# Performance work log

Hardware: AMD Instinct MI355X
Metric: run time of the kernel (lower is better)

Reference implementation:

```python
import jax, jax.numpy as jnp
import numpy as np

HIDDEN = 4096
N_HEADS = 32
N_KV_HEADS = 8
HEAD_DIM = HIDDEN // N_HEADS  # 128
GROUPS = N_HEADS // N_KV_HEADS  # 4
B, S = 1, 2048
NEG = -1e9


def setup_inputs() -> dict:
    key = jax.random.key(0)
    ks = jax.random.split(key, 8)
    hidden_states = jax.random.normal(ks[0], (B, S, HIDDEN), dtype=jnp.float32)
    # additive causal mask [B,1,S,S]
    causal = jnp.tril(jnp.ones((S, S), dtype=bool))
    attention_mask = jnp.where(causal, 0.0, NEG).astype(jnp.float32)[None, None]
    position_ids = jnp.broadcast_to(jnp.arange(S, dtype=jnp.int64), (B, S))
    inv_freq = 1.0 / (500000.0 ** (np.arange(0, HEAD_DIM, 2, dtype=np.float32) / HEAD_DIM))
    freqs = np.arange(S, dtype=np.float32)[:, None] * inv_freq[None, :]  # [S, 64]
    cos = jnp.asarray(np.cos(freqs), dtype=jnp.float32)
    sin = jnp.asarray(np.sin(freqs), dtype=jnp.float32)
    sc = 1.0 / np.sqrt(HIDDEN)
    Wq = jax.random.normal(ks[1], (HIDDEN, HIDDEN), dtype=jnp.float32) * sc
    Wk = jax.random.normal(ks[2], (N_KV_HEADS * HEAD_DIM, HIDDEN), dtype=jnp.float32) * sc
    Wv = jax.random.normal(ks[3], (N_KV_HEADS * HEAD_DIM, HIDDEN), dtype=jnp.float32) * sc
    Wo = jax.random.normal(ks[4], (HIDDEN, HIDDEN), dtype=jnp.float32) * sc
    return {"hidden_states": hidden_states, "attention_mask": attention_mask,
            "position_ids": position_ids, "cos": cos, "sin": sin,
            "Wq": Wq, "Wk": Wk, "Wv": Wv, "Wo": Wo}


def _rope(q, k, cos, sin, position_ids):
    # cos/sin: [max_pos, head_dim//2]; gather per position -> [b,1,s,hd/2]
    c = cos[position_ids][:, None]  # [b,1,s,d/2]
    s_ = sin[position_ids][:, None]
    q1, q2 = q[..., ::2], q[..., 1::2]
    k1, k2 = k[..., ::2], k[..., 1::2]
    q_rot = jnp.concatenate([q1 * c - q2 * s_, q2 * c + q1 * s_], axis=-1)
    k_rot = jnp.concatenate([k1 * c - k2 * s_, k2 * c + k1 * s_], axis=-1)
    return q_rot, k_rot


def reference(hidden_states, attention_mask, position_ids, cos, sin, Wq, Wk, Wv, Wo):
    b, s, _ = hidden_states.shape
    q = jnp.einsum('bsh,oh->bso', hidden_states, Wq).reshape(b, s, N_HEADS, HEAD_DIM).transpose(0, 2, 1, 3)
    k = jnp.einsum('bsh,oh->bso', hidden_states, Wk).reshape(b, s, N_KV_HEADS, HEAD_DIM).transpose(0, 2, 1, 3)
    v = jnp.einsum('bsh,oh->bso', hidden_states, Wv).reshape(b, s, N_KV_HEADS, HEAD_DIM).transpose(0, 2, 1, 3)
    q, k = _rope(q, k, cos, sin, position_ids)
    if GROUPS > 1:
        k = jnp.repeat(k, GROUPS, axis=1)  # [b,H,s,d]
        v = jnp.repeat(v, GROUPS, axis=1)
    scores = jnp.einsum('bhqd,bhkd->bhqk', q, k) / np.sqrt(HEAD_DIM)
    scores = scores + attention_mask
    attn = jax.nn.softmax(scores.astype(jnp.float32), axis=-1).astype(q.dtype)
    out = jnp.einsum('bhqk,bhkd->bhqd', attn, v)
    out = out.transpose(0, 2, 1, 3).reshape(b, s, HIDDEN)
    out = jnp.einsum('bso,ho->bsh', out, Wo)
    return out
```

## Files before the change

kernel.cpp:

```cpp
#include <hip/hip_runtime.h>
#include <hip/hip_bf16.h>

#define S_LEN 2048
#define HID   4096
#define NH    32
#define NKV   8
#define HD    128

typedef __attribute__((ext_vector_type(8))) short short8v;
typedef __attribute__((ext_vector_type(4))) float floatx4;

__device__ __forceinline__ float bf2f(unsigned short u) {
  union { unsigned int u32; float f; } v; v.u32 = ((unsigned int)u) << 16; return v.f;
}
__device__ __forceinline__ unsigned short f2bf(float f) {
  union { float f; unsigned int u; } v; v.f = f;
  unsigned int u = v.u + 0x7fffu + ((v.u >> 16) & 1u);
  return (unsigned short)(u >> 16);
}
__device__ __forceinline__ unsigned int cvtpk_bf16(float lo, float hi) {
  unsigned int r;
  asm("v_cvt_pk_bf16_f32 %0, %1, %2" : "=v"(r) : "v"(lo), "v"(hi));
  return r;
}

__device__ __forceinline__ void gld_lds16(const void* g, void* l) {
  __builtin_amdgcn_global_load_lds((const __attribute__((address_space(1))) void*)g,
                                   (__attribute__((address_space(3))) void*)l, 16, 0, 0);
}

__global__ __launch_bounds__(256) void cvt_all(const float* __restrict__ X,  const float* __restrict__ Wq,
                                               const float* __restrict__ Wk, const float* __restrict__ Wv,
                                               const float* __restrict__ Wo,
                                               unsigned short* __restrict__ Xb,  unsigned short* __restrict__ Wqb,
                                               unsigned short* __restrict__ Wkb, unsigned short* __restrict__ Wvb,
                                               unsigned short* __restrict__ Wob) {
  const int c0 = 1048576;
  const int c1 = c0 + 2097152;
  const int c2 = c1 + 524288;
  const int c3 = c2 + 524288;
  const int c4 = c3 + 2097152;
  int i = blockIdx.x * blockDim.x + threadIdx.x;
  int stride = gridDim.x * blockDim.x;
  for (; i < c4; i += stride) {
    const float* src; unsigned short* dst; int off;
    if (i < c0)      { src = X;  dst = Xb;  off = i; }
    else if (i < c1) { src = Wq; dst = Wqb; off = i - c0; }
    else if (i < c2) { src = Wk; dst = Wkb; off = i - c1; }
    else if (i < c3) { src = Wv; dst = Wvb; off = i - c2; }
    else             { src = Wo; dst = Wob; off = i - c3; }
    float4 v0 = ((const float4*)src)[2 * off];
    float4 v1 = ((const float4*)src)[2 * off + 1];
    union { ushort4 h[2]; uint4 u; } o;
    o.h[0].x = f2bf(v0.x); o.h[0].y = f2bf(v0.y); o.h[0].z = f2bf(v0.z); o.h[0].w = f2bf(v0.w);
    o.h[1].x = f2bf(v1.x); o.h[1].y = f2bf(v1.y); o.h[1].z = f2bf(v1.z); o.h[1].w = f2bf(v1.w);
    ((uint4*)dst)[off] = o.u;
  }
}

__global__ __launch_bounds__(512, 2) void gemm_qkv(const unsigned short* __restrict__ Xb,
                                                   const unsigned short* __restrict__ Bcat,
                                                   unsigned short* __restrict__ Qg,
                                                   unsigned short* __restrict__ Kg,
                                                   unsigned short* __restrict__ Vt) {
  __shared__ unsigned short lds[2 * 16384 + 3 * 12288];
  const int K = 4096;
  const int tid = threadIdx.x;
  const int w = tid >> 6, lane = tid & 63;
  const int fr = lane & 15, fq = lane >> 4;
  const int wm = w >> 2, wn = w & 3;
  const int brow = blockIdx.y * 256, bcol = blockIdx.x * 192;

  const int r0s = w * 32 + (lane >> 2);
  const int r1s = r0s + 16;
  const int sl0 = ((lane & 3) ^ ((r0s >> 1) & 3)) << 3;
  const int sl1 = ((lane & 3) ^ ((r1s >> 1) & 3)) << 3;
  const unsigned short* pAs0 = Xb + (size_t)(brow + r0s) * K + sl0;
  const unsigned short* pAs1 = Xb + (size_t)(brow + r1s) * K + sl1;

  const unsigned short* pBs[3];
#pragma unroll
  for (int j = 0; j < 3; ++j) {
    int c = tid + j * 512;
    int khj = (c >= 768) ? 1 : 0;
    int rowj = (c - khj * 768) >> 2;
    int slotj = c & 3;
    pBs[j] = Bcat + (size_t)(bcol + rowj) * K + khj * 32 +
             ((slotj ^ ((rowj >> 1) & 3)) << 3);
  }

  const int sl = (fq ^ ((fr >> 1) & 3)) << 3;
  int aoffb[8], boffb[3];
#pragma unroll
  for (int m = 0; m < 8; ++m) aoffb[m] = (wm * 128 + m * 16 + fr) * 32 + sl;
#pragma unroll
  for (int n = 0; n < 3; ++n) boffb[n] = (wn * 48 + n * 16 + fr) * 32 + sl;

#define STG_A(buf, kh, t)                                                     \
  do {                                                                        \
    const int ko_ = (t) * 64 + (kh) * 32;                                     \
    gld_lds16(pAs0 + ko_, lds + (buf) * 16384 + (kh) * 8192 + w * 1024);      \
    gld_lds16(pAs1 + ko_, lds + (buf) * 16384 + (kh) * 8192 + w * 1024 + 512);\
  } while (0)
#define STG_B(bb, t)                                                          \
  do {                                                                        \
    const int ko_ = (t) * 64;                                                 \
    gld_lds16(pBs[0] + ko_, lds + 32768 + (bb) * 12288 + w * 512);            \
    gld_lds16(pBs[1] + ko_, lds + 32768 + (bb) * 12288 + 4096 + w * 512);     \
    gld_lds16(pBs[2] + ko_, lds + 32768 + (bb) * 12288 + 8192 + w * 512);     \
  } while (0)

  floatx4 acc[8][3] = {};

  STG_A(0, 0, 0); STG_A(0, 1, 0); STG_B(0, 0);
  STG_A(1, 0, 1);                 STG_B(1, 1);
  asm volatile("s_waitcnt vmcnt(5)" ::: "memory");
  __builtin_amdgcn_s_barrier();

  const int NT = K / 64;
  for (int t = 0; t < NT; ++t) {
    const int c = t & 1;
    const int bb = t % 3;
    const unsigned short* LA = lds + c * 16384;
    const unsigned short* LB = lds + 32768 + bb * 12288;
    short8v a_[8], b_[3];

#pragma unroll
    for (int m = 0; m < 8; ++m) a_[m] = *(const short8v*)&LA[aoffb[m]];
#pragma unroll
    for (int n = 0; n < 3; ++n) b_[n] = *(const short8v*)&LB[boffb[n]];
    if (t + 1 < NT) STG_A(c ^ 1, 1, t + 1);
    if (t + 2 < NT) STG_B((bb + 2) % 3, t + 2);
    __builtin_amdgcn_s_setprio(1);
#pragma unroll
    for (int m = 0; m < 8; ++m)
#pragma unroll
      for (int n = 0; n < 3; ++n)
        acc[m][n] = __builtin_amdgcn_mfma_f32_16x16x32_bf16(a_[m], b_[n], acc[m][n], 0, 0, 0);
    __builtin_amdgcn_s_setprio(0);
    if (t + 2 < NT)      asm volatile("s_waitcnt vmcnt(10)" ::: "memory");
    else if (t + 1 < NT) asm volatile("s_waitcnt vmcnt(7)" ::: "memory");
    else                 asm volatile("s_waitcnt vmcnt(0)" ::: "memory");
    __builtin_amdgcn_s_barrier();

#pragma unroll
    for (int m = 0; m < 8; ++m) a_[m] = *(const short8v*)&LA[8192 + aoffb[m]];
#pragma unroll
    for (int n = 0; n < 3; ++n) b_[n] = *(const short8v*)&LB[6144 + boffb[n]];
    if (t + 2 < NT) STG_A(c, 0, t + 2);
    __builtin_amdgcn_s_setprio(1);
#pragma unroll
    for (int m = 0; m < 8; ++m)
#pragma unroll
      for (int n = 0; n < 3; ++n)
        acc[m][n] = __builtin_amdgcn_mfma_f32_16x16x32_bf16(a_[m], b_[n], acc[m][n], 0, 0, 0);
    __builtin_amdgcn_s_setprio(0);
    if (t + 2 < NT)      asm volatile("s_waitcnt vmcnt(7)" ::: "memory");
    else if (t + 1 < NT) asm volatile("s_waitcnt vmcnt(2)" ::: "memory");
    else                 asm volatile("s_waitcnt vmcnt(0)" ::: "memory");
    __builtin_amdgcn_s_barrier();
  }
#undef STG_A
#undef STG_B

  const int r0 = brow + wm * 128 + fq * 4;
#pragma unroll
  for (int m = 0; m < 8; ++m)
#pragma unroll
    for (int n = 0; n < 3; ++n) {
      const int bc = bcol + wn * 48 + n * 16;
      if (bc < 4096) {
#pragma unroll
        for (int r = 0; r < 4; ++r)
          Qg[(size_t)(r0 + m * 16 + r) * HID + bc + fr] = f2bf(acc[m][n][r]);
      } else if (bc < 5120) {
#pragma unroll
        for (int r = 0; r < 4; ++r)
          Kg[(size_t)(r0 + m * 16 + r) * 1024 + bc - 4096 + fr] = f2bf(acc[m][n][r]);
      } else {
        ushort4 pk;
        pk.x = f2bf(acc[m][n][0]); pk.y = f2bf(acc[m][n][1]);
        pk.z = f2bf(acc[m][n][2]); pk.w = f2bf(acc[m][n][3]);
        *(ushort4*)&Vt[(size_t)(bc - 5120 + fr) * S_LEN + (r0 + m * 16)] = pk;
      }
    }
}

__global__ __launch_bounds__(512, 2) void gemm_o(const unsigned short* __restrict__ Ao,
                                                 const unsigned short* __restrict__ Wob,
                                                 float* __restrict__ Out) {
  __shared__ unsigned short lds[2 * 24576];
  const int K = 4096;
  const int tid = threadIdx.x;
  const int w = tid >> 6, lane = tid & 63;
  const int fr = lane & 15, fq = lane >> 4;
  const int wm = w >> 1, wn = w & 1;
  const int brow = blockIdx.y * 256, bcol = blockIdx.x * 128;

  const int rA = tid >> 2;
  const int sA = ((tid & 3) ^ ((rA >> 1) & 3)) << 3;
  const unsigned short* pA0 = Ao  + (size_t)(brow + rA) * K + sA;
  const unsigned short* pA1 = Ao  + (size_t)(brow + 128 + rA) * K + sA;
  const unsigned short* pB0 = Wob + (size_t)(bcol + rA) * K + sA;

  const int sl = (fq ^ ((fr >> 1) & 3)) << 3;
  int aoff[4], boff[4];
#pragma unroll
  for (int m = 0; m < 4; ++m) aoff[m] = (wm * 64 + m * 16 + fr) * 32 + sl;
#pragma unroll
  for (int n = 0; n < 4; ++n) boff[n] = 16384 + (wn * 64 + n * 16 + fr) * 32 + sl;

  floatx4 acc[4][4] = {};

#define STG_KH(buf, kh, t)                                                       \
  do {                                                                           \
    const int ko_ = (t) * 64 + (kh) * 32;                                        \
    gld_lds16(pA0 + ko_, lds + (buf) * 24576 + (kh) * 8192 + w * 512);           \
    gld_lds16(pA1 + ko_, lds + (buf) * 24576 + (kh) * 8192 + 4096 + w * 512);    \
    gld_lds16(pB0 + ko_, lds + (buf) * 24576 + 16384 + (kh) * 4096 + w * 512);   \
  } while (0)

  STG_KH(0, 0, 0);
  STG_KH(0, 1, 0);
  STG_KH(1, 0, 1);
  asm volatile("s_waitcnt vmcnt(6)" ::: "memory");
  __builtin_amdgcn_s_barrier();

  const int NT = K / 64;
  for (int t = 0; t < NT; ++t) {
    const int c = t & 1;
    const unsigned short* Lc = lds + c * 24576;
    short8v a_[4], b_[4];

#pragma unroll
    for (int m = 0; m < 4; ++m) a_[m] = *(const short8v*)&Lc[aoff[m]];
#pragma unroll
    for (int n = 0; n < 4; ++n) b_[n] = *(const short8v*)&Lc[boff[n]];
    if (t + 1 < NT) STG_KH(c ^ 1, 1, t + 1);
    __builtin_amdgcn_s_setprio(1);
#pragma unroll
    for (int m = 0; m < 4; ++m)
#pragma unroll
      for (int n = 0; n < 4; ++n)
        acc[m][n] = __builtin_amdgcn_mfma_f32_16x16x32_bf16(a_[m], b_[n], acc[m][n], 0, 0, 0);
    __builtin_amdgcn_s_setprio(0);
    if (t + 1 < NT) asm volatile("s_waitcnt vmcnt(6)" ::: "memory");
    else            asm volatile("s_waitcnt vmcnt(0)" ::: "memory");
    __builtin_amdgcn_s_barrier();

#pragma unroll
    for (int m = 0; m < 4; ++m) a_[m] = *(const short8v*)&Lc[8192 + aoff[m]];
#pragma unroll
    for (int n = 0; n < 4; ++n) b_[n] = *(const short8v*)&Lc[4096 + boff[n]];
    if (t + 2 < NT) STG_KH(c, 0, t + 2);
    __builtin_amdgcn_s_setprio(1);
#pragma unroll
    for (int m = 0; m < 4; ++m)
#pragma unroll
      for (int n = 0; n < 4; ++n)
        acc[m][n] = __builtin_amdgcn_mfma_f32_16x16x32_bf16(a_[m], b_[n], acc[m][n], 0, 0, 0);
    __builtin_amdgcn_s_setprio(0);
    if (t + 2 < NT)      asm volatile("s_waitcnt vmcnt(6)" ::: "memory");
    else if (t + 1 < NT) asm volatile("s_waitcnt vmcnt(3)" ::: "memory");
    else                 asm volatile("s_waitcnt vmcnt(0)" ::: "memory");
    __builtin_amdgcn_s_barrier();
  }
#undef STG_KH

  const int r0 = brow + wm * 64 + fq * 4;
  const int c0 = bcol + wn * 64 + fr;
#pragma unroll
  for (int m = 0; m < 4; ++m)
#pragma unroll
    for (int n = 0; n < 4; ++n)
#pragma unroll
      for (int r = 0; r < 4; ++r)
        Out[(size_t)(r0 + m * 16 + r) * HID + c0 + n * 16] = acc[m][n][r];
}

__global__ __launch_bounds__(256) void rope_k(const unsigned short* __restrict__ In,
                                              const float* __restrict__ cosT,
                                              const float* __restrict__ sinT,
                                              unsigned short* __restrict__ Out) {
  int idx = blockIdx.x * 256 + threadIdx.x;
  int j = idx & 63;
  int s = (idx >> 6) & (S_LEN - 1);
  int h = idx >> 17;
  unsigned int pr = *(const unsigned int*)(In + (size_t)s * (NKV * HD) + h * HD + 2 * j);
  float k1 = bf2f((unsigned short)(pr & 0xffffu));
  float k2 = bf2f((unsigned short)(pr >> 16));
  float c = cosT[s * 64 + j], sn = sinT[s * 64 + j];
  unsigned int pk = (unsigned int)f2bf(k1 * c - k2 * sn) |
                    ((unsigned int)f2bf(k2 * c + k1 * sn) << 16);
  *(unsigned int*)(Out + ((size_t)h * S_LEN + s) * HD + 2 * j) = pk;
}

__global__ __launch_bounds__(512, 4) void attn_fwd(const unsigned short* __restrict__ Qg,
                                                   const float* __restrict__ cosT,
                                                   const float* __restrict__ sinT,
                                                   const unsigned short* __restrict__ Kr,
                                                   const unsigned short* __restrict__ Vt,
                                                   unsigned short* __restrict__ Ao) {
  __shared__ unsigned short Kl[2][64 * 128];
  __shared__ unsigned short Vl[2][128 * 64];
  const int id = blockIdx.x;
  const int xcd = id & 7, rr = id >> 3;
  const int qt = 15 - (rr >> 2);
  const int h  = xcd * 4 + (rr & 3);
  const int hk = h >> 2;
  const int qb = qt * 128;
  const int tid = threadIdx.x, w = tid >> 6, lane = tid & 63;
  const int fr = lane & 15, fq = lane >> 4;

  short8v aq[4];
  {
    const int s_row = qb + w * 16 + fr;
    const unsigned short* qp = Qg + (size_t)s_row * HID + h * HD + fq * 8;
    const float* cb = cosT + s_row * 64;
    const float* sb = sinT + s_row * 64;
    const float SC = 0.12751744f;
#pragma unroll
    for (int ks = 0; ks < 4; ++ks) {
      short8v raw = *(const short8v*)(qp + ks * 32);
      short8v ov;
#pragma unroll
      for (int e = 0; e < 4; ++e) {
        float q1 = bf2f((unsigned short)raw[2 * e]);
        float q2 = bf2f((unsigned short)raw[2 * e + 1]);
        int j = ks * 16 + fq * 4 + e;
        float c = cb[j], sn = sb[j];
        ov[2 * e]     = (short)f2bf(SC * (q1 * c - q2 * sn));
        ov[2 * e + 1] = (short)f2bf(SC * (q2 * c + q1 * sn));
      }
      aq[ks] = ov;
    }
  }

  const int kcb = ((tid & 15) * 16) ^ (((tid >> 4) & 7) << 4);
  const unsigned short* pK0 = Kr + ((size_t)hk * S_LEN + (tid >> 4)) * HD + (kcb >> 1);
  const int vcb = ((tid & 7) * 16) ^ (((tid >> 3) & 7) << 4);
  const unsigned short* pV0 = Vt + ((size_t)hk * HD + (tid >> 3)) * S_LEN + (vcb >> 1);

  const int hsel = fq >> 1;
  const int srcA = fr + ((2 * (fq & 1)) << 4);
  const int srcB = fr + ((2 * (fq & 1) + 1) << 4);

  float l_acc = 0.f;
  floatx4 o[8] = {};

#define STAGE(buf, t)                                                           \
  do {                                                                          \
    const unsigned short* pk_ = pK0 + (size_t)(t) * 64 * HD;                    \
    const unsigned short* pv_ = pV0 + (t) * 64;                                 \
    _Pragma("unroll")                                                           \
    for (int j = 0; j < 2; ++j)                                                 \
      gld_lds16(pk_ + (size_t)j * 32 * HD, &Kl[buf][j * 4096 + w * 512]);       \
    _Pragma("unroll")                                                           \
    for (int j = 0; j < 2; ++j)                                                 \
      gld_lds16(pv_ + (size_t)j * 64 * S_LEN, &Vl[buf][j * 4096 + w * 512]);    \
  } while (0)

  STAGE(0, 0);
  asm volatile("s_waitcnt vmcnt(0)" ::: "memory");
  __syncthreads();

  const int nt = 2 * qt + 2;
  int cur = 0;
  for (int t = 0; t < nt; ++t) {
    const int kv0 = t * 64;
    if (t + 1 < nt) STAGE(cur ^ 1, t + 1);

    floatx4 St[4] = {};
    const unsigned short* Kc = &Kl[cur][0];
    const unsigned short* Vc = &Vl[cur][0];
    __builtin_amdgcn_s_setprio(1);
#pragma unroll
    for (int ks = 0; ks < 4; ++ks) {
#pragma unroll
      for (int n = 0; n < 4; ++n) {
        int row = n * 16 + fr;
        int cb = (ks * 64 + fq * 16) ^ ((row & 7) << 4);
        short8v kf = *(const short8v*)&Kc[row * 128 + (cb >> 1)];
        St[n] = __builtin_amdgcn_mfma_f32_16x16x32_bf16(kf, aq[ks], St[n], 0, 0, 0);
      }
    }
    __builtin_amdgcn_s_setprio(0);

    if (t >= 2 * qt) {
#pragma unroll
      for (int n = 0; n < 4; ++n) {
#pragma unroll
        for (int r = 0; r < 4; ++r) {
          int kvg = kv0 + n * 16 + fq * 4 + r;
          if (kvg > qb + w * 16 + fr) St[n][r] = -1e30f;
        }
      }
    }

    unsigned int pk[4][2];
#pragma unroll
    for (int n = 0; n < 4; ++n) {
      float p0 = exp2f(St[n][0]);
      float p1 = exp2f(St[n][1]);
      float p2 = exp2f(St[n][2]);
      float p3 = exp2f(St[n][3]);
      l_acc += (p0 + p1) + (p2 + p3);
      pk[n][0] = cvtpk_bf16(p0, p1);
      pk[n][1] = cvtpk_bf16(p2, p3);
    }

    short8v pa[2];
#pragma unroll
    for (int ks = 0; ks < 2; ++ks) {
      unsigned int v0a = __shfl(pk[2 * ks][0], srcA), v0b = __shfl(pk[2 * ks + 1][0], srcA);
      unsigned int v1a = __shfl(pk[2 * ks][1], srcA), v1b = __shfl(pk[2 * ks + 1][1], srcA);
      unsigned int v2a = __shfl(pk[2 * ks][0], srcB), v2b = __shfl(pk[2 * ks + 1][0], srcB);
      unsigned int v3a = __shfl(pk[2 * ks][1], srcB), v3b = __shfl(pk[2 * ks + 1][1], srcB);
      uint4 u;
      u.x = hsel ? v0b : v0a;
      u.y = hsel ? v1b : v1a;
      u.z = hsel ? v2b : v2a;
      u.w = hsel ? v3b : v3a;
      pa[ks] = *(short8v*)&u;
    }

    __builtin_amdgcn_s_setprio(1);
#pragma unroll
    for (int nf = 0; nf < 8; ++nf) {
#pragma unroll
      for (int ks = 0; ks < 2; ++ks) {
        int row = nf * 16 + fr;
        int cb = (ks * 64 + fq * 16) ^ ((row & 7) << 4);
        short8v bv = *(const short8v*)&Vc[row * 64 + (cb >> 1)];
        o[nf] = __builtin_amdgcn_mfma_f32_16x16x32_bf16(pa[ks], bv, o[nf], 0, 0, 0);
      }
    }
    __builtin_amdgcn_s_setprio(0);

    if (t + 1 < nt) {
      asm volatile("s_waitcnt vmcnt(0)" ::: "memory");
      __syncthreads();
      cur ^= 1;
    }
  }
#undef STAGE

  float L = l_acc;
  L += __shfl_xor(L, 16);
  L += __shfl_xor(L, 32);
  float rinv[4];
#pragma unroll
  for (int r = 0; r < 4; ++r) rinv[r] = 1.0f / __shfl(L, fq * 4 + r);

  unsigned short* aop = Ao + (size_t)(qb + w * 16 + fq * 4) * HID + h * HD + fr;
#pragma unroll
  for (int nf = 0; nf < 8; ++nf)
#pragma unroll
    for (int r = 0; r < 4; ++r)
      aop[(size_t)r * HID + nf * 16] = f2bf(o[nf][r] * rinv[r]);
}

extern "C" void kernel_launch(void* const* d_in, const int* in_sizes, int n_in,
                              void* d_out, int out_size, void* d_ws, size_t ws_size,
                              hipStream_t stream) {
  (void)in_sizes; (void)n_in; (void)out_size; (void)ws_size;
  const float* X    = (const float*)d_in[0];
  const float* cosT = (const float*)d_in[3];
  const float* sinT = (const float*)d_in[4];
  const float* Wq   = (const float*)d_in[5];
  const float* Wk   = (const float*)d_in[6];
  const float* Wv   = (const float*)d_in[7];
  const float* Wo   = (const float*)d_in[8];

  char* ws = (char*)d_ws;
  size_t off = 0;
  auto alloc = [&](size_t bytes) { char* p = ws + off; off += (bytes + 255) & ~(size_t)255; return p; };
  unsigned short* Xb  = (unsigned short*)alloc((size_t)S_LEN * HID * 2);
  unsigned short* Wqb = (unsigned short*)alloc((size_t)HID * HID * 2);
  unsigned short* Wkb = (unsigned short*)alloc((size_t)1024 * HID * 2);
  unsigned short* Wvb = (unsigned short*)alloc((size_t)1024 * HID * 2);
  unsigned short* Wob = (unsigned short*)alloc((size_t)HID * HID * 2);
  unsigned short* Qg  = (unsigned short*)alloc((size_t)S_LEN * HID * 2);
  unsigned short* Kg  = (unsigned short*)alloc((size_t)S_LEN * 1024 * 2);
  unsigned short* Vt  = (unsigned short*)alloc((size_t)1024 * S_LEN * 2);
  unsigned short* Kr = Wqb;
  unsigned short* Ao = Xb;

  cvt_all<<<2048, 256, 0, stream>>>(X, Wq, Wk, Wv, Wo, Xb, Wqb, Wkb, Wvb, Wob);
  gemm_qkv<<<dim3(32, 8), 512, 0, stream>>>(Xb, Wqb, Qg, Kg, Vt);
  rope_k<<<(NKV * S_LEN * 64) / 256, 256, 0, stream>>>(Kg, cosT, sinT, Kr);
  attn_fwd<<<512, 512, 0, stream>>>(Qg, cosT, sinT, Kr, Vt, Ao);
  gemm_o<<<dim3(32, 8), 512, 0, stream>>>(Ao, Wob, (float*)d_out);
}
```

Before: 289.3 us.

## Halve QKV GEMM row tile to 128 and simplify to double-buffered pipeline

The QKV projection GEMM tile shrinks from 256x192 to 128x192, doubling the grid to 512 blocks. The A/B staging moves from a staggered 3-deep B ring to a plain double buffer that prefetches the whole next k-tile, and launch bounds are raised so more blocks can be resident per CU. The aim is to fill the MI355X's CUs better, since 256 blocks underfill them, and to shrink LDS per block. The cost is lower arithmetic intensity per block, more total B-operand traffic, and a shallower prefetch pipeline.

```diff
diff --git a/kernel.cpp b/kernel.cpp
--- a/kernel.cpp
+++ b/kernel.cpp
@@ -58,114 +58,107 @@
   }
 }
 
-__global__ __launch_bounds__(512, 2) void gemm_qkv(const unsigned short* __restrict__ Xb,
+__global__ __launch_bounds__(512, 4) void gemm_qkv(const unsigned short* __restrict__ Xb,
                                                    const unsigned short* __restrict__ Bcat,
                                                    unsigned short* __restrict__ Qg,
                                                    unsigned short* __restrict__ Kg,
                                                    unsigned short* __restrict__ Vt) {
-  __shared__ unsigned short lds[2 * 16384 + 3 * 12288];
+  __shared__ unsigned short lds[40960];
   const int K = 4096;
   const int tid = threadIdx.x;
   const int w = tid >> 6, lane = tid & 63;
   const int fr = lane & 15, fq = lane >> 4;
   const int wm = w >> 2, wn = w & 3;
-  const int brow = blockIdx.y * 256, bcol = blockIdx.x * 192;
-
-  const int r0s = w * 32 + (lane >> 2);
-  const int r1s = r0s + 16;
-  const int sl0 = ((lane & 3) ^ ((r0s >> 1) & 3)) << 3;
-  const int sl1 = ((lane & 3) ^ ((r1s >> 1) & 3)) << 3;
-  const unsigned short* pAs0 = Xb + (size_t)(brow + r0s) * K + sl0;
-  const unsigned short* pAs1 = Xb + (size_t)(brow + r1s) * K + sl1;
+  const int brow = blockIdx.y * 128, bcol = blockIdx.x * 192;
+
+  const int rA = tid >> 2, sA = tid & 3;
+  const unsigned short* pA = Xb + (size_t)(brow + rA) * K + ((sA ^ ((rA >> 1) & 3)) << 3);
 
   const unsigned short* pBs[3];
 #pragma unroll
   for (int j = 0; j < 3; ++j) {
     int c = tid + j * 512;
     int khj = (c >= 768) ? 1 : 0;
-    int rowj = (c - khj * 768) >> 2;
-    int slotj = c & 3;
+    int rem = c - khj * 768;
+    int rowj = rem >> 2;
+    int slotj = rem & 3;
     pBs[j] = Bcat + (size_t)(bcol + rowj) * K + khj * 32 +
              ((slotj ^ ((rowj >> 1) & 3)) << 3);
   }
 
   const int sl = (fq ^ ((fr >> 1) & 3)) << 3;
-  int aoffb[8], boffb[3];
-#pragma unroll
-  for (int m = 0; m < 8; ++m) aoffb[m] = (wm * 128 + m * 16 + fr) * 32 + sl;
+  int aoffb[4], boffb[3];
+#pragma unroll
+  for (int m = 0; m < 4; ++m) aoffb[m] = (wm * 64 + m * 16 + fr) * 32 + sl;
 #pragma unroll
   for (int n = 0; n < 3; ++n) boffb[n] = (wn * 48 + n * 16 + fr) * 32 + sl;
 
 #define STG_A(buf, kh, t)                                                     \
+  gld_lds16(pA + (t) * 64 + (kh) * 32, lds + (buf) * 8192 + (kh) * 4096 + w * 512)
+#define STG_B(buf, t)                                                         \
   do {                                                                        \
-    const int ko_ = (t) * 64 + (kh) * 32;                                     \
-    gld_lds16(pAs0 + ko_, lds + (buf) * 16384 + (kh) * 8192 + w * 1024);      \
-    gld_lds16(pAs1 + ko_, lds + (buf) * 16384 + (kh) * 8192 + w * 1024 + 512);\
+    gld_lds16(pBs[0] + (t) * 64, lds + 16384 + (buf) * 12288 + w * 512);      \
+    gld_lds16(pBs[1] + (t) * 64, lds + 16384 + (buf) * 12288 + 4096 + w * 512); \
+    gld_lds16(pBs[2] + (t) * 64, lds + 16384 + (buf) * 12288 + 8192 + w * 512); \
   } while (0)
-#define STG_B(bb, t)                                                          \
-  do {                                                                        \
-    const int ko_ = (t) * 64;                                                 \
-    gld_lds16(pBs[0] + ko_, lds + 32768 + (bb) * 12288 + w * 512);            \
-    gld_lds16(pBs[1] + ko_, lds + 32768 + (bb) * 12288 + 4096 + w * 512);     \
-    gld_lds16(pBs[2] + ko_, lds + 32768 + (bb) * 12288 + 8192 + w * 512);     \
-  } while (0)
-
-  floatx4 acc[8][3] = {};
-
-  STG_A(0, 0, 0); STG_A(0, 1, 0); STG_B(0, 0);
-  STG_A(1, 0, 1);                 STG_B(1, 1);
-  asm volatile("s_waitcnt vmcnt(5)" ::: "memory");
+
+  floatx4 acc[4][3] = {};
+
+  STG_A(0, 0, 0);
+  STG_B(0, 0);
+  STG_A(0, 1, 0);
+  asm volatile("s_waitcnt vmcnt(1)" ::: "memory");
   __builtin_amdgcn_s_barrier();
 
   const int NT = K / 64;
   for (int t = 0; t < NT; ++t) {
     const int c = t & 1;
-    const int bb = t % 3;
-    const unsigned short* LA = lds + c * 16384;
-    const unsigned short* LB = lds + 32768 + bb * 12288;
-    short8v a_[8], b_[3];
-
-#pragma unroll
-    for (int m = 0; m < 8; ++m) a_[m] = *(const short8v*)&LA[aoffb[m]];
+    const unsigned short* LA = lds + c * 8192;
+    const unsigned short* LB = lds + 16384 + c * 12288;
+    short8v a_[4], b_[3];
+
+#pragma unroll
+    for (int m = 0; m < 4; ++m) a_[m] = *(const short8v*)&LA[aoffb[m]];
 #pragma unroll
     for (int n = 0; n < 3; ++n) b_[n] = *(const short8v*)&LB[boffb[n]];
-    if (t + 1 < NT) STG_A(c ^ 1, 1, t + 1);
-    if (t + 2 < NT) STG_B((bb + 2) % 3, t + 2);
-    __builtin_amdgcn_s_setprio(1);
-#pragma unroll
-    for (int m = 0; m < 8; ++m)
+    if (t + 1 < NT) {
+      STG_A(c ^ 1, 0, t + 1);
+      STG_B(c ^ 1, t + 1);
+      STG_A(c ^ 1, 1, t + 1);
+    }
+    __builtin_amdgcn_s_setprio(1);
+#pragma unroll
+    for (int m = 0; m < 4; ++m)
 #pragma unroll
       for (int n = 0; n < 3; ++n)
         acc[m][n] = __builtin_amdgcn_mfma_f32_16x16x32_bf16(a_[m], b_[n], acc[m][n], 0, 0, 0);
     __builtin_amdgcn_s_setprio(0);
-    if (t + 2 < NT)      asm volatile("s_waitcnt vmcnt(10)" ::: "memory");
-    else if (t + 1 < NT) asm volatile("s_waitcnt vmcnt(7)" ::: "memory");
-    else                 asm volatile("s_waitcnt vmcnt(0)" ::: "memory");
+    if (t + 1 < NT) asm volatile("s_waitcnt vmcnt(5)" ::: "memory");
+    else            asm volatile("s_waitcnt vmcnt(0)" ::: "memory");
     __builtin_amdgcn_s_barrier();
 
 #pragma unroll
-    for (int m = 0; m < 8; ++m) a_[m] = *(const short8v*)&LA[8192 + aoffb[m]];
+    for (int m = 0; m < 4; ++m) a_[m] = *(const short8v*)&LA[4096 + aoffb[m]];
 #pragma unroll
     for (int n = 0; n < 3; ++n) b_[n] = *(const short8v*)&LB[6144 + boffb[n]];
-    if (t + 2 < NT) STG_A(c, 0, t + 2);
-    __builtin_amdgcn_s_setprio(1);
-#pragma unroll
-    for (int m = 0; m < 8; ++m)
+    __builtin_amdgcn_s_setprio(1);
+#pragma unroll
+    for (int m = 0; m < 4; ++m)
 #pragma unroll
       for (int n = 0; n < 3; ++n)
         acc[m][n] = __builtin_amdgcn_mfma_f32_16x16x32_bf16(a_[m], b_[n], acc[m][n], 0, 0, 0);
     __builtin_amdgcn_s_setprio(0);
-    if (t + 2 < NT)      asm volatile("s_waitcnt vmcnt(7)" ::: "memory");
-    else if (t + 1 < NT) asm volatile("s_waitcnt vmcnt(2)" ::: "memory");
-    else                 asm volatile("s_waitcnt vmcnt(0)" ::: "memory");
-    __builtin_amdgcn_s_barrier();
+    if (t + 1 < NT) {
+      asm volatile("s_waitcnt vmcnt(1)" ::: "memory");
+      __builtin_amdgcn_s_barrier();
+    }
   }
 #undef STG_A
 #undef STG_B
 
-  const int r0 = brow + wm * 128 + fq * 4;
-#pragma unroll
-  for (int m = 0; m < 8; ++m)
+  const int r0 = brow + wm * 64 + fq * 4;
+#pragma unroll
+  for (int m = 0; m < 4; ++m)
 #pragma unroll
     for (int n = 0; n < 3; ++n) {
       const int bc = bcol + wn * 48 + n * 16;
@@ -487,7 +480,7 @@
   unsigned short* Ao = Xb;
 
   cvt_all<<<2048, 256, 0, stream>>>(X, Wq, Wk, Wv, Wo, Xb, Wqb, Wkb, Wvb, Wob);
-  gemm_qkv<<<dim3(32, 8), 512, 0, stream>>>(Xb, Wqb, Qg, Kg, Vt);
+  gemm_qkv<<<dim3(32, 16), 512, 0, stream>>>(Xb, Wqb, Qg, Kg, Vt);
   rope_k<<<(NKV * S_LEN * 64) / 256, 256, 0, stream>>>(Kg, cosT, sinT, Kr);
   attn_fwd<<<512, 512, 0, stream>>>(Qg, cosT, sinT, Kr, Vt, Ao);
   gemm_o<<<dim3(32, 8), 512, 0, stream>>>(Ao, Wob, (float*)d_out);
```

Result: slower. 300.8 us (+4.0%).

## Triple-buffer gemm_o LDS pipeline with one barrier per K-tile

Applied to the files above, without the earlier changes.

Restructures the output-projection GEMM from a double-buffered, half-tile staged loop with two barriers per 64-wide K step into a three-stage LDS ring. Loads are issued two tiles ahead and the loop uses one barrier per iteration. The intent is to cut barrier and wait stalls and give global loads more time to land. In exchange LDS use grows from 96KB to 144KB per block, which may lower the number of resident blocks below the launch bound of 2 and raise register pressure from holding both K-halves of fragments.

```diff
diff --git a/kernel.cpp b/kernel.cpp
--- a/kernel.cpp
+++ b/kernel.cpp
@@ -189,7 +189,7 @@
 __global__ __launch_bounds__(512, 2) void gemm_o(const unsigned short* __restrict__ Ao,
                                                  const unsigned short* __restrict__ Wob,
                                                  float* __restrict__ Out) {
-  __shared__ unsigned short lds[2 * 24576];
+  __shared__ unsigned short lds[73728];
   const int K = 4096;
   const int tid = threadIdx.x;
   const int w = tid >> 6, lane = tid & 63;
@@ -208,62 +208,62 @@
 #pragma unroll
   for (int m = 0; m < 4; ++m) aoff[m] = (wm * 64 + m * 16 + fr) * 32 + sl;
 #pragma unroll
-  for (int n = 0; n < 4; ++n) boff[n] = 16384 + (wn * 64 + n * 16 + fr) * 32 + sl;
+  for (int n = 0; n < 4; ++n) boff[n] = (wn * 64 + n * 16 + fr) * 32 + sl;
 
   floatx4 acc[4][4] = {};
 
 #define STG_KH(buf, kh, t)                                                       \
   do {                                                                           \
     const int ko_ = (t) * 64 + (kh) * 32;                                        \
-    gld_lds16(pA0 + ko_, lds + (buf) * 24576 + (kh) * 8192 + w * 512);           \
-    gld_lds16(pA1 + ko_, lds + (buf) * 24576 + (kh) * 8192 + 4096 + w * 512);    \
-    gld_lds16(pB0 + ko_, lds + (buf) * 24576 + 16384 + (kh) * 4096 + w * 512);   \
+    gld_lds16(pA0 + ko_, lds + (buf) * 16384 + (kh) * 8192 + w * 512);           \
+    gld_lds16(pA1 + ko_, lds + (buf) * 16384 + (kh) * 8192 + 4096 + w * 512);    \
+    gld_lds16(pB0 + ko_, lds + 49152 + (buf) * 8192 + (kh) * 4096 + w * 512);    \
   } while (0)
 
-  STG_KH(0, 0, 0);
-  STG_KH(0, 1, 0);
-  STG_KH(1, 0, 1);
+  STG_KH(0, 0, 0); STG_KH(0, 1, 0);
+  STG_KH(1, 0, 1); STG_KH(1, 1, 1);
   asm volatile("s_waitcnt vmcnt(6)" ::: "memory");
   __builtin_amdgcn_s_barrier();
 
   const int NT = K / 64;
+  int a3 = 0;
   for (int t = 0; t < NT; ++t) {
-    const int c = t & 1;
-    const unsigned short* Lc = lds + c * 24576;
-    short8v a_[4], b_[4];
-
-#pragma unroll
-    for (int m = 0; m < 4; ++m) a_[m] = *(const short8v*)&Lc[aoff[m]];
-#pragma unroll
-    for (int n = 0; n < 4; ++n) b_[n] = *(const short8v*)&Lc[boff[n]];
-    if (t + 1 < NT) STG_KH(c ^ 1, 1, t + 1);
+    const unsigned short* LA = lds + a3 * 16384;
+    const unsigned short* LB = lds + 49152 + a3 * 8192;
+    short8v a0_[4], b0_[4], a1_[4], b1_[4];
+
+#pragma unroll
+    for (int m = 0; m < 4; ++m) a0_[m] = *(const short8v*)&LA[aoff[m]];
+#pragma unroll
+    for (int n = 0; n < 4; ++n) b0_[n] = *(const short8v*)&LB[boff[n]];
+#pragma unroll
+    for (int m = 0; m < 4; ++m) a1_[m] = *(const short8v*)&LA[8192 + aoff[m]];
+#pragma unroll
+    for (int n = 0; n < 4; ++n) b1_[n] = *(const short8v*)&LB[4096 + boff[n]];
+
+    if (t + 2 < NT) {
+      const int nb = (a3 + 2 >= 3) ? a3 - 1 : a3 + 2;
+      STG_KH(nb, 0, t + 2);
+      STG_KH(nb, 1, t + 2);
+    }
+
     __builtin_amdgcn_s_setprio(1);
 #pragma unroll
     for (int m = 0; m < 4; ++m)
 #pragma unroll
       for (int n = 0; n < 4; ++n)
-        acc[m][n] = __builtin_amdgcn_mfma_f32_16x16x32_bf16(a_[m], b_[n], acc[m][n], 0, 0, 0);
+        acc[m][n] = __builtin_amdgcn_mfma_f32_16x16x32_bf16(a0_[m], b0_[n], acc[m][n], 0, 0, 0);
+#pragma unroll
+    for (int m = 0; m < 4; ++m)
+#pragma unroll
+      for (int n = 0; n < 4; ++n)
+        acc[m][n] = __builtin_amdgcn_mfma_f32_16x16x32_bf16(a1_[m], b1_[n], acc[m][n], 0, 0, 0);
     __builtin_amdgcn_s_setprio(0);
-    if (t + 1 < NT) asm volatile("s_waitcnt vmcnt(6)" ::: "memory");
-    else            asm volatile("s_waitcnt vmcnt(0)" ::: "memory");
-    __builtin_amdgcn_s_barrier();
-
-#pragma unroll
-    for (int m = 0; m < 4; ++m) a_[m] = *(const short8v*)&Lc[8192 + aoff[m]];
-#pragma unroll
-    for (int n = 0; n < 4; ++n) b_[n] = *(const short8v*)&Lc[4096 + boff[n]];
-    if (t + 2 < NT) STG_KH(c, 0, t + 2);
-    __builtin_amdgcn_s_setprio(1);
-#pragma unroll
-    for (int m = 0; m < 4; ++m)
-#pragma unroll
-      for (int n = 0; n < 4; ++n)
-        acc[m][n] = __builtin_amdgcn_mfma_f32_16x16x32_bf16(a_[m], b_[n], acc[m][n], 0, 0, 0);
-    __builtin_amdgcn_s_setprio(0);
+
     if (t + 2 < NT)      asm volatile("s_waitcnt vmcnt(6)" ::: "memory");
-    else if (t + 1 < NT) asm volatile("s_waitcnt vmcnt(3)" ::: "memory");
-    else                 asm volatile("s_waitcnt vmcnt(0)" ::: "memory");
-    __builtin_amdgcn_s_barrier();
+    else if (t + 1 < NT) asm volatile("s_waitcnt vmcnt(0)" ::: "memory");
+    if (t + 1 < NT) __builtin_amdgcn_s_barrier();
+    a3 = (a3 == 2) ? 0 : a3 + 1;
   }
 #undef STG_KH
 
```

After: 285.4 us (median of 2 runs). About the same (-1.4%).
